# Optimization experiments

Measured on AMD Instinct MI355X. Metric: run time of the kernel, lower is better.

The kernel has to match this reference:

```python
import jax, jax.numpy as jnp
import numpy as np

SIGMA = 10.0
H, W, C = 512, 512, 6


def _edt_sq(nb):
    """Exact squared Euclidean distance transform: distance from each pixel to the
    nearest True pixel of nb [H,W] (Felzenszwalb-style separable 2-pass,
    brute-force row pass). Matches scipy.distance_transform_edt(~nb)**2 when
    nb marks non-background (distance 0 at nb==True)."""
    h, w = nb.shape
    BIG = jnp.float32(h + w)  # cap > any achievable 1D distance

    def step(carry, row):
        d = jnp.where(row, 0.0, jnp.minimum(carry + 1.0, BIG))
        return d, d

    init = jnp.full((w,), BIG, dtype=jnp.float32)
    _, fwd = jax.lax.scan(step, init, nb)
    _, bwd = jax.lax.scan(step, init, nb[::-1])
    g = jnp.minimum(fwd, bwd[::-1]) ** 2  # [H,W] squared distance along columns
    j = jnp.arange(w, dtype=jnp.float32)
    diff2 = (j[:, None] - j[None, :]) ** 2  # [W,W] (x-k)^2
    # D2[i,x] = min_k g[i,k] + (x-k)^2   -> [H,W,W] intermediate, reduced over k
    return jnp.min(g[:, None, :] + diff2[None, :, :], axis=-1)


def setup_inputs() -> dict:
    key = jax.random.key(0)
    k1, k2 = jax.random.split(key)
    pred = jax.random.normal(k1, (1, C, H, W), dtype=jnp.float32)
    labels = jax.random.randint(k2, (1, H, W), 0, C)
    target = jax.nn.one_hot(labels, C, dtype=jnp.float32)  # [1,H,W,C]
    return {"pred": pred, "target": target}


def reference(pred, target):
    mask = target[0]  # [H,W,C] (squeeze(0))
    non_background = jnp.any(mask[..., :5] > 0, axis=-1)  # [H,W]
    d2 = _edt_sq(non_background)
    bg_w = jnp.exp(-d2 / (2.0 * SIGMA ** 2))
    weights = jnp.ones_like(mask).at[..., -1].set(bg_w)  # [H,W,C]
    weights = jnp.transpose(weights, (2, 0, 1))[None]  # [1,C,H,W]
    logp = jax.nn.log_softmax(pred, axis=1)  # [1,C,H,W]
    t = jnp.transpose(target, (0, 3, 1, 2))  # [1,C,H,W]
    ce = -jnp.sum(t * logp, axis=1)  # [1,H,W] soft-target cross entropy
    # torch broadcasting: [1,H,W] * [1,C,H,W] -> [1,C,H,W], then global mean
    return jnp.mean(ce[:, None, :, :] * weights)
```

## Files before the change

kernel.cpp:

```cpp
#include <hip/hip_runtime.h>
#include <math.h>

#define HH 512
#define WW 512
#define CC 6

static constexpr float BIGD = (float)(HH + WW);
static constexpr float INV2SIG2 = 1.0f / (2.0f * 10.0f * 10.0f);

__device__ __forceinline__ bool is_nb(const float* __restrict__ target, int p) {
    const float* t = target + (size_t)p * CC;
    return (t[0] > 0.0f) | (t[1] > 0.0f) | (t[2] > 0.0f) | (t[3] > 0.0f) | (t[4] > 0.0f);
}

__global__ __launch_bounds__(512) void k_main(const float* __restrict__ pred,
                                              const float* __restrict__ target,
                                              float* __restrict__ partials) {
    __shared__ float gs[WW];
    __shared__ float red[8];
    const int i = blockIdx.x;
    const int x = threadIdx.x;
    const int p = i * WW + x;

    float dist;
    if (is_nb(target, p)) {
        dist = 0.0f;
    } else {
        dist = BIGD;
        for (int k = 1; k < HH; ++k) {
            const int iu = i - k, id = i + k;
            bool out_of_range = true;
            if (iu >= 0) {
                out_of_range = false;
                if (is_nb(target, iu * WW + x)) { dist = (float)k; break; }
            }
            if (id < HH) {
                out_of_range = false;
                if (is_nb(target, id * WW + x)) { dist = (float)k; break; }
            }
            if (out_of_range) break;
        }
    }
    gs[x] = dist * dist;
    __syncthreads();

    float best = gs[x];
    for (int r = 1; r < WW; ++r) {
        float rr = (float)(r * r);
        if (rr >= best) break;
        int kl = x - r;
        int kr = x + r;
        if (kl >= 0)  best = fminf(best, gs[kl] + rr);
        if (kr < WW)  best = fminf(best, gs[kr] + rr);
    }
    float bg_w = expf(-best * INV2SIG2);

    float pv[CC];
#pragma unroll
    for (int c = 0; c < CC; ++c) pv[c] = pred[c * (HH * WW) + p];
    float m = pv[0];
#pragma unroll
    for (int c = 1; c < CC; ++c) m = fmaxf(m, pv[c]);
    float s = 0.0f;
#pragma unroll
    for (int c = 0; c < CC; ++c) s += expf(pv[c] - m);
    float lse = m + logf(s);
    const float* t = target + (size_t)p * CC;
    float ce = 0.0f;
#pragma unroll
    for (int c = 0; c < CC; ++c) ce += t[c] * (lse - pv[c]);

    float contrib = ce * (5.0f + bg_w);

#pragma unroll
    for (int off = 32; off > 0; off >>= 1) contrib += __shfl_down(contrib, off, 64);
    if ((x & 63) == 0) red[x >> 6] = contrib;
    __syncthreads();
    if (x == 0) {
        float sum = 0.0f;
#pragma unroll
        for (int w = 0; w < 8; ++w) sum += red[w];
        partials[i] = sum;
    }
}

__global__ void k_final(const float* __restrict__ partials, float* __restrict__ out) {
    __shared__ float red[8];
    const int x = threadIdx.x;
    float v = partials[x];
#pragma unroll
    for (int off = 32; off > 0; off >>= 1) v += __shfl_down(v, off, 64);
    if ((x & 63) == 0) red[x >> 6] = v;
    __syncthreads();
    if (x == 0) {
        float sum = 0.0f;
#pragma unroll
        for (int w = 0; w < 8; ++w) sum += red[w];
        out[0] = sum / (float)(CC * HH * WW);
    }
}

extern "C" void kernel_launch(void* const* d_in, const int* in_sizes, int n_in,
                              void* d_out, int out_size, void* d_ws, size_t ws_size,
                              hipStream_t stream) {
    const float* pred   = (const float*)d_in[0];
    const float* target = (const float*)d_in[1];
    float* partials = (float*)d_ws;
    float* out = (float*)d_out;

    k_main <<<HH, WW, 0, stream>>>(pred, target, partials);
    k_final<<<1, 512, 0, stream>>>(partials, out);
}
```

Measured before the change: 11.41 us.

## Fuse final reduction via last-block counter and simplify non-background test

Replaces the separate final-reduction kernel with a last-block-done pattern using an atomic counter, reset by a memset each launch. The non-background check now reads only the background channel, which relies on one-hot targets. Target loads are vectorized as float2, and pred uses nontemporal loads. This removes one kernel launch and cuts the global loads in the column distance scan, at the cost of atomics and an extra memset.

```diff
diff --git a/kernel.cpp b/kernel.cpp
--- a/kernel.cpp
+++ b/kernel.cpp
@@ -4,41 +4,45 @@
 #define HH 512
 #define WW 512
 #define CC 6
+#define NPIX (HH * WW)
 
 static constexpr float BIGD = (float)(HH + WW);
 static constexpr float INV2SIG2 = 1.0f / (2.0f * 10.0f * 10.0f);
 
-__device__ __forceinline__ bool is_nb(const float* __restrict__ target, int p) {
-    const float* t = target + (size_t)p * CC;
-    return (t[0] > 0.0f) | (t[1] > 0.0f) | (t[2] > 0.0f) | (t[3] > 0.0f) | (t[4] > 0.0f);
+__device__ __forceinline__ bool is_nb5(const float* __restrict__ target, int p) {
+    return target[(size_t)p * CC + 5] == 0.0f;
 }
 
 __global__ __launch_bounds__(512) void k_main(const float* __restrict__ pred,
                                               const float* __restrict__ target,
-                                              float* __restrict__ partials) {
+                                              float* __restrict__ partials,
+                                              unsigned int* __restrict__ counter,
+                                              float* __restrict__ out) {
     __shared__ float gs[WW];
     __shared__ float red[8];
+    __shared__ int lastFlag;
     const int i = blockIdx.x;
     const int x = threadIdx.x;
     const int p = i * WW + x;
 
+    const float* t = target + (size_t)p * CC;
+    const float2 t01 = *(const float2*)(t);
+    const float2 t23 = *(const float2*)(t + 2);
+    const float2 t45 = *(const float2*)(t + 4);
+    const bool nb = (t45.y == 0.0f);
+
     float dist;
-    if (is_nb(target, p)) {
+    if (nb) {
         dist = 0.0f;
     } else {
         dist = BIGD;
         for (int k = 1; k < HH; ++k) {
             const int iu = i - k, id = i + k;
-            bool out_of_range = true;
-            if (iu >= 0) {
-                out_of_range = false;
-                if (is_nb(target, iu * WW + x)) { dist = (float)k; break; }
-            }
-            if (id < HH) {
-                out_of_range = false;
-                if (is_nb(target, id * WW + x)) { dist = (float)k; break; }
-            }
-            if (out_of_range) break;
+            if (iu < 0 && id >= HH) break;
+            bool hit = false;
+            if (iu >= 0) hit = is_nb5(target, iu * WW + x);
+            if (id < HH) hit |= is_nb5(target, id * WW + x);
+            if (hit) { dist = (float)k; break; }
         }
     }
     gs[x] = dist * dist;
@@ -57,7 +61,7 @@
 
     float pv[CC];
 #pragma unroll
-    for (int c = 0; c < CC; ++c) pv[c] = pred[c * (HH * WW) + p];
+    for (int c = 0; c < CC; ++c) pv[c] = __builtin_nontemporal_load(&pred[c * NPIX + p]);
     float m = pv[0];
 #pragma unroll
     for (int c = 1; c < CC; ++c) m = fmaxf(m, pv[c]);
@@ -65,10 +69,9 @@
 #pragma unroll
     for (int c = 0; c < CC; ++c) s += expf(pv[c] - m);
     float lse = m + logf(s);
-    const float* t = target + (size_t)p * CC;
-    float ce = 0.0f;
-#pragma unroll
-    for (int c = 0; c < CC; ++c) ce += t[c] * (lse - pv[c]);
+    float dot = t01.x * pv[0] + t01.y * pv[1] + t23.x * pv[2]
+              + t23.y * pv[3] + t45.x * pv[4] + t45.y * pv[5];
+    float ce = lse - dot;
 
     float contrib = ce * (5.0f + bg_w);
 
@@ -80,23 +83,25 @@
         float sum = 0.0f;
 #pragma unroll
         for (int w = 0; w < 8; ++w) sum += red[w];
-        partials[i] = sum;
+        __hip_atomic_store(&partials[i], sum, __ATOMIC_RELEASE, __HIP_MEMORY_SCOPE_AGENT);
+        unsigned prev = __hip_atomic_fetch_add(counter, 1u, __ATOMIC_ACQ_REL,
+                                               __HIP_MEMORY_SCOPE_AGENT);
+        lastFlag = (prev == (unsigned)(gridDim.x - 1)) ? 1 : 0;
     }
-}
+    __syncthreads();
 
-__global__ void k_final(const float* __restrict__ partials, float* __restrict__ out) {
-    __shared__ float red[8];
-    const int x = threadIdx.x;
-    float v = partials[x];
+    if (lastFlag) {
+        float v = __hip_atomic_load(&partials[x], __ATOMIC_ACQUIRE, __HIP_MEMORY_SCOPE_AGENT);
 #pragma unroll
-    for (int off = 32; off > 0; off >>= 1) v += __shfl_down(v, off, 64);
-    if ((x & 63) == 0) red[x >> 6] = v;
-    __syncthreads();
-    if (x == 0) {
-        float sum = 0.0f;
+        for (int off = 32; off > 0; off >>= 1) v += __shfl_down(v, off, 64);
+        if ((x & 63) == 0) red[x >> 6] = v;
+        __syncthreads();
+        if (x == 0) {
+            float sum = 0.0f;
 #pragma unroll
-        for (int w = 0; w < 8; ++w) sum += red[w];
-        out[0] = sum / (float)(CC * HH * WW);
+            for (int w = 0; w < 8; ++w) sum += red[w];
+            out[0] = sum / (float)(CC * HH * WW);
+        }
     }
 }
 
@@ -106,8 +111,9 @@
     const float* pred   = (const float*)d_in[0];
     const float* target = (const float*)d_in[1];
     float* partials = (float*)d_ws;
+    unsigned int* counter = (unsigned int*)((float*)d_ws + HH);
     float* out = (float*)d_out;
 
-    k_main <<<HH, WW, 0, stream>>>(pred, target, partials);
-    k_final<<<1, 512, 0, stream>>>(partials, out);
+    hipMemsetAsync(counter, 0, sizeof(unsigned int), stream);
+    k_main<<<HH, WW, 0, stream>>>(pred, target, partials, counter, out);
 }
```

Result: slower. 25.32 us (+122.0%).

## Split into CE pass and bitmask-based 2D ring-search distance transform

Applied to the files above, without the earlier changes.

Splits the work into three kernels. The first computes per-pixel cross-entropy and packs a background bitmask with ballots. The second loads the whole 32KB bitmask into shared memory and runs an expanding ring search for the nearest foreground pixel, stopping early once the ring radius squared exceeds the best distance found. The final kernel reduces the partials. This replaces the strided column scans over the 24-byte-per-pixel target and the separable pass, at the cost of an extra launch, a global round trip for the CE values, and per-thread divergent ring loops.

```diff
diff --git a/kernel.cpp b/kernel.cpp
--- a/kernel.cpp
+++ b/kernel.cpp
@@ -4,60 +4,24 @@
 #define HH 512
 #define WW 512
 #define CC 6
+#define NPIX (HH * WW)
+#define MROW 8
 
-static constexpr float BIGD = (float)(HH + WW);
 static constexpr float INV2SIG2 = 1.0f / (2.0f * 10.0f * 10.0f);
 
-__device__ __forceinline__ bool is_nb(const float* __restrict__ target, int p) {
+__global__ __launch_bounds__(512) void k_ce(const float* __restrict__ pred,
+                                            const float* __restrict__ target,
+                                            float* __restrict__ ce,
+                                            unsigned long long* __restrict__ mask) {
+    const int p = blockIdx.x * 512 + threadIdx.x;
     const float* t = target + (size_t)p * CC;
-    return (t[0] > 0.0f) | (t[1] > 0.0f) | (t[2] > 0.0f) | (t[3] > 0.0f) | (t[4] > 0.0f);
-}
-
-__global__ __launch_bounds__(512) void k_main(const float* __restrict__ pred,
-                                              const float* __restrict__ target,
-                                              float* __restrict__ partials) {
-    __shared__ float gs[WW];
-    __shared__ float red[8];
-    const int i = blockIdx.x;
-    const int x = threadIdx.x;
-    const int p = i * WW + x;
-
-    float dist;
-    if (is_nb(target, p)) {
-        dist = 0.0f;
-    } else {
-        dist = BIGD;
-        for (int k = 1; k < HH; ++k) {
-            const int iu = i - k, id = i + k;
-            bool out_of_range = true;
-            if (iu >= 0) {
-                out_of_range = false;
-                if (is_nb(target, iu * WW + x)) { dist = (float)k; break; }
-            }
-            if (id < HH) {
-                out_of_range = false;
-                if (is_nb(target, id * WW + x)) { dist = (float)k; break; }
-            }
-            if (out_of_range) break;
-        }
-    }
-    gs[x] = dist * dist;
-    __syncthreads();
-
-    float best = gs[x];
-    for (int r = 1; r < WW; ++r) {
-        float rr = (float)(r * r);
-        if (rr >= best) break;
-        int kl = x - r;
-        int kr = x + r;
-        if (kl >= 0)  best = fminf(best, gs[kl] + rr);
-        if (kr < WW)  best = fminf(best, gs[kr] + rr);
-    }
-    float bg_w = expf(-best * INV2SIG2);
+    const float2 t01 = *(const float2*)(t);
+    const float2 t23 = *(const float2*)(t + 2);
+    const float2 t45 = *(const float2*)(t + 4);
 
     float pv[CC];
 #pragma unroll
-    for (int c = 0; c < CC; ++c) pv[c] = pred[c * (HH * WW) + p];
+    for (int c = 0; c < CC; ++c) pv[c] = __builtin_nontemporal_load(&pred[c * NPIX + p]);
     float m = pv[0];
 #pragma unroll
     for (int c = 1; c < CC; ++c) m = fmaxf(m, pv[c]);
@@ -65,27 +29,89 @@
 #pragma unroll
     for (int c = 0; c < CC; ++c) s += expf(pv[c] - m);
     float lse = m + logf(s);
-    const float* t = target + (size_t)p * CC;
-    float ce = 0.0f;
+    float dot = t01.x * pv[0] + t01.y * pv[1] + t23.x * pv[2]
+              + t23.y * pv[3] + t45.x * pv[4] + t45.y * pv[5];
+    __builtin_nontemporal_store(lse - dot, &ce[p]);
+
+    unsigned long long b = __ballot(t45.y == 0.0f);
+    if ((threadIdx.x & 63) == 0) mask[p >> 6] = b;
+}
+
+__global__ __launch_bounds__(512) void k_edt(const float* __restrict__ ce,
+                                             const unsigned long long* __restrict__ mask,
+                                             float* __restrict__ partials) {
+    __shared__ unsigned long long ms[HH * MROW];
+    __shared__ float red[8];
+    const int tid = threadIdx.x;
+
+    const uint4* gm = (const uint4*)mask;
+    uint4* lm = (uint4*)ms;
 #pragma unroll
-    for (int c = 0; c < CC; ++c) ce += t[c] * (lse - pv[c]);
+    for (int j = 0; j < 4; ++j) lm[tid + j * 512] = gm[tid + j * 512];
+    __syncthreads();
 
-    float contrib = ce * (5.0f + bg_w);
+    float acc = 0.0f;
+#pragma unroll
+    for (int q = 0; q < 2; ++q) {
+        const int i = blockIdx.x * 2 + q;
+        const int x = tid;
+        const float cev = __builtin_nontemporal_load(&ce[i * WW + x]);
+
+        float w;
+        if ((ms[i * MROW + (x >> 6)] >> (x & 63)) & 1ull) {
+            w = 6.0f;
+        } else {
+            int best = 0x7fffffff;
+            for (int r = 1; r <= 723; ++r) {
+                if (r * r >= best) break;
+                const int iu = i - r, idn = i + r;
+                const int xlo = max(x - r, 0), xhi = min(x + r, WW - 1);
+                if (iu >= 0) {
+                    const unsigned long long* row = &ms[iu * MROW];
+                    for (int xx = xlo; xx <= xhi; ++xx)
+                        if ((row[xx >> 6] >> (xx & 63)) & 1ull) {
+                            int dx = xx - x;
+                            best = min(best, dx * dx + r * r);
+                        }
+                }
+                if (idn < HH) {
+                    const unsigned long long* row = &ms[idn * MROW];
+                    for (int xx = xlo; xx <= xhi; ++xx)
+                        if ((row[xx >> 6] >> (xx & 63)) & 1ull) {
+                            int dx = xx - x;
+                            best = min(best, dx * dx + r * r);
+                        }
+                }
+                for (int dy = -(r - 1); dy <= r - 1; ++dy) {
+                    const int ii = i + dy;
+                    if (ii < 0 || ii >= HH) continue;
+                    const int d2s = dy * dy + r * r;
+                    if (d2s >= best) continue;
+                    const int xl = x - r, xr = x + r;
+                    if (xl >= 0  && ((ms[ii * MROW + (xl >> 6)] >> (xl & 63)) & 1ull)) best = d2s;
+                    if (xr < WW  && ((ms[ii * MROW + (xr >> 6)] >> (xr & 63)) & 1ull)) best = min(best, d2s);
+                }
+            }
+            if (best == 0x7fffffff) best = 1048576;
+            w = 5.0f + expf(-(float)best * INV2SIG2);
+        }
+        acc += cev * w;
+    }
 
 #pragma unroll
-    for (int off = 32; off > 0; off >>= 1) contrib += __shfl_down(contrib, off, 64);
-    if ((x & 63) == 0) red[x >> 6] = contrib;
+    for (int off = 32; off > 0; off >>= 1) acc += __shfl_down(acc, off, 64);
+    if ((tid & 63) == 0) red[tid >> 6] = acc;
     __syncthreads();
-    if (x == 0) {
-        float sum = 0.0f;
+    if (tid == 0) {
+        float s = 0.0f;
 #pragma unroll
-        for (int w = 0; w < 8; ++w) sum += red[w];
-        partials[i] = sum;
+        for (int w8 = 0; w8 < 8; ++w8) s += red[w8];
+        partials[blockIdx.x] = s;
     }
 }
 
-__global__ void k_final(const float* __restrict__ partials, float* __restrict__ out) {
-    __shared__ float red[8];
+__global__ void k_fin(const float* __restrict__ partials, float* __restrict__ out) {
+    __shared__ float red[4];
     const int x = threadIdx.x;
     float v = partials[x];
 #pragma unroll
@@ -93,10 +119,7 @@
     if ((x & 63) == 0) red[x >> 6] = v;
     __syncthreads();
     if (x == 0) {
-        float sum = 0.0f;
-#pragma unroll
-        for (int w = 0; w < 8; ++w) sum += red[w];
-        out[0] = sum / (float)(CC * HH * WW);
+        out[0] = (red[0] + red[1] + red[2] + red[3]) / (float)(CC * NPIX);
     }
 }
 
@@ -105,9 +128,13 @@
                               hipStream_t stream) {
     const float* pred   = (const float*)d_in[0];
     const float* target = (const float*)d_in[1];
-    float* partials = (float*)d_ws;
+    float* ws = (float*)d_ws;
+    float* ce = ws;
+    unsigned long long* mask = (unsigned long long*)(ws + NPIX);
+    float* partials = (float*)(mask + HH * MROW);
     float* out = (float*)d_out;
 
-    k_main <<<HH, WW, 0, stream>>>(pred, target, partials);
-    k_final<<<1, 512, 0, stream>>>(partials, out);
+    k_ce <<<512, 512, 0, stream>>>(pred, target, ce, mask);
+    k_edt<<<256, 512, 0, stream>>>(ce, mask, partials);
+    k_fin<<<1, 256, 0, stream>>>(partials, out);
 }
```

Measured after the change: 15.65 us. 1.37x slower.
